# Performance work log

Measured on AMD Instinct MI355X. Metric: run time of the kernel, lower is better.

The kernel has to match this reference:

```python
import jax, jax.numpy as jnp
import numpy as np

B, Z, NOBS = 16384, 64, 2
D = Z + NOBS  # update_mlp_in_size
H1, H2 = 16, 16
HC1, HC2 = 32, 32


def setup_inputs() -> dict:
    key = jax.random.key(0)
    ks = jax.random.split(key, 20)
    inp = {}
    inp['latents'] = jax.random.normal(ks[0], (B, Z), jnp.float32)
    inp['obs'] = jax.random.normal(ks[1], (B, NOBS), jnp.float32)
    # reparameterization noise (torch.randn_like equivalents, made explicit)
    inp['noise_update'] = jax.random.normal(ks[2], (B, D, Z), jnp.float32)
    inp['noise_global'] = jax.random.normal(ks[3], (B, Z), jnp.float32)
    # parameters
    inp['z_0'] = jax.random.normal(ks[4], (Z,), jnp.float32)
    inp['mult_u'] = jnp.ones((D, Z), jnp.float32)
    inp['logvar_u'] = jax.random.uniform(ks[5], (D, Z), jnp.float32, -3.0, -2.0)
    inp['mult_g'] = jnp.ones((Z,), jnp.float32)
    inp['logvar_g'] = jax.random.uniform(ks[6], (Z,), jnp.float32, -3.0, -2.0)
    # per-latent update MLPs, batched over Z
    s = lambda fan_in: 1.0 / np.sqrt(fan_in)
    inp['W1'] = jax.random.uniform(ks[7], (Z, D, H1), jnp.float32, -s(D), s(D))
    inp['b1'] = jax.random.uniform(ks[8], (Z, H1), jnp.float32, -s(D), s(D))
    inp['W2'] = jax.random.uniform(ks[9], (Z, H1, H2), jnp.float32, -s(H1), s(H1))
    inp['b2'] = jax.random.uniform(ks[10], (Z, H2), jnp.float32, -s(H1), s(H1))
    inp['W3'] = jax.random.uniform(ks[11], (Z, H2, 2), jnp.float32, -s(H2), s(H2))
    inp['b3'] = jax.random.uniform(ks[12], (Z, 2), jnp.float32, -s(H2), s(H2))
    # choice MLP (include_stimulus=False -> input dim Z)
    inp['Wc1'] = jax.random.uniform(ks[13], (Z, HC1), jnp.float32, -s(Z), s(Z))
    inp['bc1'] = jax.random.uniform(ks[14], (HC1,), jnp.float32, -s(Z), s(Z))
    inp['Wc2'] = jax.random.uniform(ks[15], (HC1, HC2), jnp.float32, -s(HC1), s(HC1))
    inp['bc2'] = jax.random.uniform(ks[16], (HC2,), jnp.float32, -s(HC1), s(HC1))
    inp['Wc3'] = jax.random.uniform(ks[17], (HC2, 2), jnp.float32, -s(HC2), s(HC2))
    inp['bc3'] = jax.random.uniform(ks[18], (2,), jnp.float32, -s(HC2), s(HC2))
    inp['t_0'] = 0  # False
    return inp


def reference(latents, obs, noise_update, noise_global, z_0, mult_u, logvar_u,
              mult_g, logvar_g, W1, b1, W2, b2, W3, b3,
              Wc1, bc1, Wc2, bc2, Wc3, bc3, t_0):
    lat = jnp.broadcast_to(z_0, latents.shape) if t_0 else latents  # [B,Z]
    x = jnp.concatenate([lat, obs], axis=-1)  # [B,D]
    # --- per-latent update bottlenecks, vectorized over Z ---
    var_u = jnp.exp(logvar_u)                      # [D,Z]
    mean_u = x[:, :, None] * mult_u[None]          # [B,D,Z]
    kld_u = -0.5 * jnp.sum(1.0 + logvar_u[None] - mean_u ** 2 - var_u[None], axis=1)  # [B,Z]
    x_tilde = noise_update * jnp.sqrt(var_u)[None] + mean_u  # [B,D,Z]
    # --- per-latent tiny MLPs, batched as grouped GEMMs ---
    h = jax.nn.relu(jnp.einsum('bdz,zdh->bzh', x_tilde, W1) + b1[None])
    h = jax.nn.relu(jnp.einsum('bzh,zhk->bzk', h, W2) + b2[None])
    o = jnp.einsum('bzk,zko->bzo', h, W3) + b3[None]          # [B,Z,2]
    u = o[..., 0]
    w = jax.nn.sigmoid(o[..., 1])
    new_latents = (1.0 - w) * lat + u * w          # gated update, [B,Z]
    # --- global bottleneck ---
    var_g = jnp.exp(logvar_g)
    mean_g = mult_g * new_latents
    kld_g = -0.5 * jnp.sum(1.0 + logvar_g - mean_g ** 2 - var_g, axis=-1)  # [B]
    z_tilde = noise_global * jnp.sqrt(var_g) + mean_g
    # --- choice MLP (no stimulus) ---
    y = jax.nn.relu(z_tilde @ Wc1 + bc1)
    y = jax.nn.relu(y @ Wc2 + bc2)
    y = y @ Wc3 + bc3                              # [B,2]
    return (y, z_tilde, kld_g, kld_u)
```

## Files before the change

### kernel.cpp

```cpp
#include <hip/hip_runtime.h>
#include <stdint.h>

#define BB 16384
#define ZZ 64
#define DD 66
#define NB 4
#define WPB 4
#define ROWS (WPB*NB)

#define OFF_SVMU 0
#define OFF_C0U  8448
#define OFF_MG   8512
#define OFF_SVG  8576
#define OFF_C0G  8640
#define OFF_W1T  8704
#define OFF_W2T  76288
#define OFF_W3T  92672

__global__ void prep_kernel(const float* __restrict__ mult_u, const float* __restrict__ logvar_u,
                            const float* __restrict__ mult_g, const float* __restrict__ logvar_g,
                            const float* __restrict__ W1, const float* __restrict__ W2,
                            const float* __restrict__ W3, float* __restrict__ ws) {
  const int d = blockIdx.x;
  const int t = threadIdx.x;
  const int z = t >> 2, q = t & 3;

  {
    const float4 v = *reinterpret_cast<const float4*>(W1 + (z*DD + d)*16 + q*4);
    *reinterpret_cast<float4*>(ws + OFF_W1T + ((d*4 + q)*64 + z)*4) = v;
  }
  if (t < ZZ) {
    ws[OFF_SVMU + 2*(d*ZZ + t)]     = mult_u[d*ZZ + t];
    ws[OFF_SVMU + 2*(d*ZZ + t) + 1] = __expf(0.5f * logvar_u[d*ZZ + t]);
  }
  if (d < 16) {
    const float4 v = *reinterpret_cast<const float4*>(W2 + (z*16 + d)*16 + q*4);
    *reinterpret_cast<float4*>(ws + OFF_W2T + ((d*4 + q)*64 + z)*4) = v;
  }
  if (d == 16 || d == 17) {
    const int idx = (d - 16)*256 + t;
    const int qq = idx >> 6, zz = idx & 63;
    const float4 v = *reinterpret_cast<const float4*>(W3 + zz*32 + qq*4);
    *reinterpret_cast<float4*>(ws + OFF_W3T + (qq*64 + zz)*4) = v;
  }
  if (d == 0) {
    if (t < ZZ) {
      float s = 0.f;
      for (int dd = 0; dd < DD; ++dd) {
        const float lv = logvar_u[dd*ZZ + t];
        s += 1.f + lv - __expf(lv);
      }
      ws[OFF_C0U + t] = -0.5f * s;
      ws[OFF_MG  + t] = mult_g[t];
      ws[OFF_SVG + t] = __expf(0.5f * logvar_g[t]);
    }
    if (t == 0) {
      float s = 0.f;
      for (int zc = 0; zc < ZZ; ++zc) {
        const float lv = logvar_g[zc];
        s += 1.f + lv - __expf(lv);
      }
      ws[OFF_C0G] = -0.5f * s;
    }
  }
}

__global__ __launch_bounds__(256, 1)
void disrnn_main(const float* __restrict__ latents, const float* __restrict__ obs,
                 const float* __restrict__ noise_u, const float* __restrict__ noise_g,
                 const float* __restrict__ z0, const float* __restrict__ b1,
                 const float* __restrict__ b2, const float* __restrict__ b3,
                 const float* __restrict__ Wc1, const float* __restrict__ bc1,
                 const float* __restrict__ Wc2, const float* __restrict__ bc2,
                 const float* __restrict__ Wc3, const float* __restrict__ bc3,
                 const float* __restrict__ ws, const int* __restrict__ t0p,
                 float* __restrict__ out) {
  float* out_zt = out + BB*2;
  float* out_kg = out + BB*2 + BB*ZZ;
  float* out_ku = out + BB*2 + BB*ZZ + BB;

  __shared__ float x_lds[WPB][NB][68];
  __shared__ float ztl[ROWS][64];
  __shared__ float y1[ROWS][32];
  __shared__ float y2[ROWS][32];

  const int tid  = threadIdx.x;
  const int w    = tid >> 6;
  const int lane = tid & 63;
  const int b0   = (blockIdx.x * WPB + w) * NB;
  const int t0   = *t0p;

#pragma unroll
  for (int i = 0; i < NB; ++i) {
    x_lds[w][i][lane] = t0 ? z0[lane] : latents[(b0 + i)*ZZ + lane];
    if (lane < 2) x_lds[w][i][ZZ + lane] = obs[(b0 + i)*2 + lane];
  }
  __syncthreads();

  const float c0u_l = ws[OFF_C0U + lane];
  const float mg_l  = ws[OFF_MG + lane];
  const float svg_l = ws[OFF_SVG + lane];
  const float c0g   = ws[OFF_C0G];

  float acc[NB][16], kacc[NB];
  {
    const float4* bp = reinterpret_cast<const float4*>(b1 + lane*16);
    float b1r[16];
#pragma unroll
    for (int q = 0; q < 4; ++q) {
      const float4 v = bp[q];
      b1r[4*q] = v.x; b1r[4*q+1] = v.y; b1r[4*q+2] = v.z; b1r[4*q+3] = v.w;
    }
#pragma unroll
    for (int i = 0; i < NB; ++i) {
      kacc[i] = 0.f;
#pragma unroll
      for (int h = 0; h < 16; ++h) acc[i][h] = b1r[h];
    }
  }

  const float*  w1t  = ws + OFF_W1T;
  const float2* svmu = reinterpret_cast<const float2*>(ws + OFF_SVMU);
  const float* np[NB];
#pragma unroll
  for (int i = 0; i < NB; ++i) np[i] = noise_u + (b0 + i)*DD*ZZ + lane;

  float nv_c[NB], nv_n[NB];
#pragma unroll
  for (int i = 0; i < NB; ++i) { nv_c[i] = np[i][0]; nv_n[i] = np[i][ZZ]; }
  float wv_c[16];
#pragma unroll
  for (int q = 0; q < 4; ++q) {
    const float4 v = *reinterpret_cast<const float4*>(w1t + (q*64 + lane)*4);
    wv_c[4*q] = v.x; wv_c[4*q+1] = v.y; wv_c[4*q+2] = v.z; wv_c[4*q+3] = v.w;
  }
  float2 sm_c = svmu[lane];
  float xv_c[NB];
#pragma unroll
  for (int i = 0; i < NB; ++i) xv_c[i] = x_lds[w][i][0];

#pragma unroll 2
  for (int d = 0; d < DD; ++d) {
    const int dn  = (d + 1 < DD) ? d + 1 : DD - 1;
    const int dnn = (d + 2 < DD) ? d + 2 : DD - 1;
    float nv2[NB];
#pragma unroll
    for (int i = 0; i < NB; ++i) nv2[i] = np[i][dnn*ZZ];
    float wv_n[16];
#pragma unroll
    for (int q = 0; q < 4; ++q) {
      const float4 v = *reinterpret_cast<const float4*>(w1t + ((dn*4 + q)*64 + lane)*4);
      wv_n[4*q] = v.x; wv_n[4*q+1] = v.y; wv_n[4*q+2] = v.z; wv_n[4*q+3] = v.w;
    }
    const float2 sm_n = svmu[dn*ZZ + lane];
    float xv_n[NB];
#pragma unroll
    for (int i = 0; i < NB; ++i) xv_n[i] = x_lds[w][i][dn];

#pragma unroll
    for (int i = 0; i < NB; ++i) {
      const float mean = xv_c[i] * sm_c.x;
      kacc[i] = fmaf(mean, mean, kacc[i]);
      const float xt = fmaf(nv_c[i], sm_c.y, mean);
#pragma unroll
      for (int h = 0; h < 16; ++h) acc[i][h] = fmaf(xt, wv_c[h], acc[i][h]);
    }
#pragma unroll
    for (int i = 0; i < NB; ++i) { nv_c[i] = nv_n[i]; nv_n[i] = nv2[i]; xv_c[i] = xv_n[i]; }
#pragma unroll
    for (int h = 0; h < 16; ++h) wv_c[h] = wv_n[h];
    sm_c = sm_n;
  }

  float h2[NB][16];
  {
    const float4* bp = reinterpret_cast<const float4*>(b2 + lane*16);
    float b2r[16];
#pragma unroll
    for (int q = 0; q < 4; ++q) {
      const float4 v = bp[q];
      b2r[4*q] = v.x; b2r[4*q+1] = v.y; b2r[4*q+2] = v.z; b2r[4*q+3] = v.w;
    }
#pragma unroll
    for (int i = 0; i < NB; ++i) {
#pragma unroll
      for (int h = 0; h < 16; ++h) acc[i][h] = fmaxf(acc[i][h], 0.f);
#pragma unroll
      for (int k = 0; k < 16; ++k) h2[i][k] = b2r[k];
    }
  }
  const float* w2t = ws + OFF_W2T;
#pragma unroll
  for (int h = 0; h < 16; ++h) {
    float wv2[16];
#pragma unroll
    for (int q = 0; q < 4; ++q) {
      const float4 v = *reinterpret_cast<const float4*>(w2t + ((h*4 + q)*64 + lane)*4);
      wv2[4*q] = v.x; wv2[4*q+1] = v.y; wv2[4*q+2] = v.z; wv2[4*q+3] = v.w;
    }
#pragma unroll
    for (int i = 0; i < NB; ++i) {
      const float hv = acc[i][h];
#pragma unroll
      for (int k = 0; k < 16; ++k) h2[i][k] = fmaf(hv, wv2[k], h2[i][k]);
    }
  }

  float w3r[32];
  {
    const float* w3t = ws + OFF_W3T;
#pragma unroll
    for (int q = 0; q < 8; ++q) {
      const float4 v = *reinterpret_cast<const float4*>(w3t + (q*64 + lane)*4);
      w3r[4*q] = v.x; w3r[4*q+1] = v.y; w3r[4*q+2] = v.z; w3r[4*q+3] = v.w;
    }
  }
  const float2 b3v = reinterpret_cast<const float2*>(b3)[lane];
#pragma unroll
  for (int i = 0; i < NB; ++i) {
    const int b = b0 + i;
    float o0 = b3v.x, o1 = b3v.y;
#pragma unroll
    for (int k = 0; k < 16; ++k) {
      const float hv = fmaxf(h2[i][k], 0.f);
      o0 = fmaf(hv, w3r[2*k], o0);
      o1 = fmaf(hv, w3r[2*k + 1], o1);
    }
    const float xl = x_lds[w][i][lane];
    const float wg = 1.f / (1.f + __expf(-o1));
    const float nl = fmaf(wg, o0 - xl, xl);
    const float tg = mg_l * nl;
    const float zt = fmaf(noise_g[b*ZZ + lane], svg_l, tg);
    out_zt[b*ZZ + lane] = zt;
    out_ku[b*ZZ + lane] = fmaf(0.5f, kacc[i], c0u_l);
    ztl[w*NB + i][lane] = zt;
    float t2 = tg * tg;
#pragma unroll
    for (int off = 32; off; off >>= 1) t2 += __shfl_xor(t2, off);
    if (lane == 0) out_kg[b] = fmaf(0.5f, t2, c0g);
  }
  __syncthreads();

  const int r  = tid >> 5;
  const int hc = tid & 31;
#pragma unroll
  for (int g = 0; g < 2; ++g) {
    const int row = g*8 + r;
    float a = bc1[hc];
#pragma unroll
    for (int zc = 0; zc < 64; ++zc) a = fmaf(ztl[row][zc], Wc1[zc*32 + hc], a);
    y1[row][hc] = fmaxf(a, 0.f);
  }
  __syncthreads();
#pragma unroll
  for (int g = 0; g < 2; ++g) {
    const int row = g*8 + r;
    float a = bc2[hc];
#pragma unroll
    for (int k = 0; k < 32; ++k) a = fmaf(y1[row][k], Wc2[k*32 + hc], a);
    y2[row][hc] = fmaxf(a, 0.f);
  }
  __syncthreads();
  if (tid < ROWS*2) {
    const int rr = tid >> 1, o = tid & 1;
    float s = bc3[o];
#pragma unroll
    for (int k = 0; k < 32; ++k) s = fmaf(y2[rr][k], Wc3[2*k + o], s);
    out[(blockIdx.x*ROWS + rr)*2 + o] = s;
  }
}

extern "C" void kernel_launch(void* const* d_in, const int* in_sizes, int n_in,
                              void* d_out, int out_size, void* d_ws, size_t ws_size,
                              hipStream_t stream) {
  (void)in_sizes; (void)n_in; (void)out_size; (void)ws_size;
  const float* latents  = (const float*)d_in[0];
  const float* obs      = (const float*)d_in[1];
  const float* noise_u  = (const float*)d_in[2];
  const float* noise_g  = (const float*)d_in[3];
  const float* z0       = (const float*)d_in[4];
  const float* mult_u   = (const float*)d_in[5];
  const float* logvar_u = (const float*)d_in[6];
  const float* mult_g   = (const float*)d_in[7];
  const float* logvar_g = (const float*)d_in[8];
  const float* W1       = (const float*)d_in[9];
  const float* b1       = (const float*)d_in[10];
  const float* W2       = (const float*)d_in[11];
  const float* b2       = (const float*)d_in[12];
  const float* W3       = (const float*)d_in[13];
  const float* b3       = (const float*)d_in[14];
  const float* Wc1      = (const float*)d_in[15];
  const float* bc1      = (const float*)d_in[16];
  const float* Wc2      = (const float*)d_in[17];
  const float* bc2      = (const float*)d_in[18];
  const float* Wc3      = (const float*)d_in[19];
  const float* bc3      = (const float*)d_in[20];
  const int*  t0p       = (const int*)d_in[21];
  float* ws   = (float*)d_ws;
  float* outp = (float*)d_out;

  prep_kernel<<<66, 256, 0, stream>>>(mult_u, logvar_u, mult_g, logvar_g, W1, W2, W3, ws);
  disrnn_main<<<BB/ROWS, 256, 0, stream>>>(latents, obs, noise_u, noise_g, z0,
                                           b1, b2, b3, Wc1, bc1, Wc2, bc2, Wc3, bc3,
                                           ws, t0p, outp);
}
```

Measured before the change: 503.0 us.

## Stage noise tiles through double-buffered LDS with float4 global loads

Replaces the per-lane scalar noise loads (one 4-byte load per d per row) with wide float4 loads that fetch four d-rows of noise at once. Each chunk is written into a per-wave double-buffered LDS region, then read back as scalars in the compute loop. The main d-loop is restructured into 16 chunks of 4 plus a 2-iteration tail. This cuts the number of global load instructions for the dominant noise stream, at the cost of extra LDS traffic, more LDS usage, and a bounds branch on the prefetch.

New measurement: 500.9 us. No clear change (-0.4%).

```diff
diff --git a/kernel.cpp b/kernel.cpp
--- a/kernel.cpp
+++ b/kernel.cpp
@@ -80,6 +80,7 @@
   float* out_ku = out + BB*2 + BB*ZZ + BB;
 
   __shared__ float x_lds[WPB][NB][68];
+  __shared__ float noise_lds[WPB][2][NB][4*ZZ];
   __shared__ float ztl[ROWS][64];
   __shared__ float y1[ROWS][32];
   __shared__ float y2[ROWS][32];
@@ -121,13 +122,20 @@
 
   const float*  w1t  = ws + OFF_W1T;
   const float2* svmu = reinterpret_cast<const float2*>(ws + OFF_SVMU);
-  const float* np[NB];
-#pragma unroll
-  for (int i = 0; i < NB; ++i) np[i] = noise_u + (b0 + i)*DD*ZZ + lane;
-
-  float nv_c[NB], nv_n[NB];
-#pragma unroll
-  for (int i = 0; i < NB; ++i) { nv_c[i] = np[i][0]; nv_n[i] = np[i][ZZ]; }
+
+  const int dsub = lane >> 4;
+  float4 st[NB];
+  {
+#pragma unroll
+    for (int i = 0; i < NB; ++i)
+      st[i] = *reinterpret_cast<const float4*>(
+          noise_u + ((size_t)(b0 + i)*DD + 0)*ZZ + lane*4);
+#pragma unroll
+    for (int i = 0; i < NB; ++i)
+      *reinterpret_cast<float4*>(&noise_lds[w][0][i][lane*4]) = st[i];
+  }
+  int cur = 0;
+
   float wv_c[16];
 #pragma unroll
   for (int q = 0; q < 4; ++q) {
@@ -139,37 +147,90 @@
 #pragma unroll
   for (int i = 0; i < NB; ++i) xv_c[i] = x_lds[w][i][0];
 
-#pragma unroll 2
-  for (int d = 0; d < DD; ++d) {
-    const int dn  = (d + 1 < DD) ? d + 1 : DD - 1;
-    const int dnn = (d + 2 < DD) ? d + 2 : DD - 1;
-    float nv2[NB];
-#pragma unroll
-    for (int i = 0; i < NB; ++i) nv2[i] = np[i][dnn*ZZ];
-    float wv_n[16];
-#pragma unroll
-    for (int q = 0; q < 4; ++q) {
-      const float4 v = *reinterpret_cast<const float4*>(w1t + ((dn*4 + q)*64 + lane)*4);
-      wv_n[4*q] = v.x; wv_n[4*q+1] = v.y; wv_n[4*q+2] = v.z; wv_n[4*q+3] = v.w;
-    }
-    const float2 sm_n = svmu[dn*ZZ + lane];
-    float xv_n[NB];
-#pragma unroll
-    for (int i = 0; i < NB; ++i) xv_n[i] = x_lds[w][i][dn];
-
-#pragma unroll
-    for (int i = 0; i < NB; ++i) {
-      const float mean = xv_c[i] * sm_c.x;
-      kacc[i] = fmaf(mean, mean, kacc[i]);
-      const float xt = fmaf(nv_c[i], sm_c.y, mean);
-#pragma unroll
-      for (int h = 0; h < 16; ++h) acc[i][h] = fmaf(xt, wv_c[h], acc[i][h]);
-    }
-#pragma unroll
-    for (int i = 0; i < NB; ++i) { nv_c[i] = nv_n[i]; nv_n[i] = nv2[i]; xv_c[i] = xv_n[i]; }
-#pragma unroll
-    for (int h = 0; h < 16; ++h) wv_c[h] = wv_n[h];
-    sm_c = sm_n;
+  for (int c = 0; c < 16; ++c) {
+    {
+      const int d0n = (c + 1) * 4;
+#pragma unroll
+      for (int i = 0; i < NB; ++i) {
+        st[i] = make_float4(0.f, 0.f, 0.f, 0.f);
+        if (d0n + dsub < DD)
+          st[i] = *reinterpret_cast<const float4*>(
+              noise_u + ((size_t)(b0 + i)*DD + d0n)*ZZ + lane*4);
+      }
+    }
+    float nvv[4][NB];
+#pragma unroll
+    for (int j = 0; j < 4; ++j)
+#pragma unroll
+      for (int i = 0; i < NB; ++i)
+        nvv[j][i] = noise_lds[w][cur][i][j*ZZ + lane];
+
+#pragma unroll
+    for (int j = 0; j < 4; ++j) {
+      const int d  = c*4 + j;
+      const int dn = d + 1;
+      float wv_n[16];
+#pragma unroll
+      for (int q = 0; q < 4; ++q) {
+        const float4 v = *reinterpret_cast<const float4*>(w1t + ((dn*4 + q)*64 + lane)*4);
+        wv_n[4*q] = v.x; wv_n[4*q+1] = v.y; wv_n[4*q+2] = v.z; wv_n[4*q+3] = v.w;
+      }
+      const float2 sm_n = svmu[dn*ZZ + lane];
+      float xv_n[NB];
+#pragma unroll
+      for (int i = 0; i < NB; ++i) xv_n[i] = x_lds[w][i][dn];
+#pragma unroll
+      for (int i = 0; i < NB; ++i) {
+        const float mean = xv_c[i] * sm_c.x;
+        kacc[i] = fmaf(mean, mean, kacc[i]);
+        const float xt = fmaf(nvv[j][i], sm_c.y, mean);
+#pragma unroll
+        for (int h = 0; h < 16; ++h) acc[i][h] = fmaf(xt, wv_c[h], acc[i][h]);
+      }
+#pragma unroll
+      for (int h = 0; h < 16; ++h) wv_c[h] = wv_n[h];
+      sm_c = sm_n;
+#pragma unroll
+      for (int i = 0; i < NB; ++i) xv_c[i] = xv_n[i];
+    }
+#pragma unroll
+    for (int i = 0; i < NB; ++i)
+      *reinterpret_cast<float4*>(&noise_lds[w][cur ^ 1][i][lane*4]) = st[i];
+    cur ^= 1;
+  }
+
+  {
+    float nvt[2][NB];
+#pragma unroll
+    for (int j = 0; j < 2; ++j)
+#pragma unroll
+      for (int i = 0; i < NB; ++i)
+        nvt[j][i] = noise_lds[w][cur][i][j*ZZ + lane];
+#pragma unroll
+    for (int j = 0; j < 2; ++j) {
+      const int d  = 64 + j;
+      const int dn = (d + 1 < DD) ? d + 1 : DD - 1;
+      float wv_n[16];
+#pragma unroll
+      for (int q = 0; q < 4; ++q) {
+        const float4 v = *reinterpret_cast<const float4*>(w1t + ((dn*4 + q)*64 + lane)*4);
+        wv_n[4*q] = v.x; wv_n[4*q+1] = v.y; wv_n[4*q+2] = v.z; wv_n[4*q+3] = v.w;
+      }
+      const float2 sm_n = svmu[dn*ZZ + lane];
+#pragma unroll
+      for (int i = 0; i < NB; ++i) {
+        const float mean = xv_c[i] * sm_c.x;
+        kacc[i] = fmaf(mean, mean, kacc[i]);
+        const float xt = fmaf(nvt[j][i], sm_c.y, mean);
+#pragma unroll
+        for (int h = 0; h < 16; ++h) acc[i][h] = fmaf(xt, wv_c[h], acc[i][h]);
+      }
+#pragma unroll
+      for (int h = 0; h < 16; ++h) wv_c[h] = wv_n[h];
+      sm_c = sm_n;
+#pragma unroll
+      for (int i = 0; i < NB; ++i) xv_c[i] = x_lds[w][i][dn];
+    }
   }
 
   float h2[NB][16];
```

## Stage W1 and noise-scale weights through double-buffered LDS chunks

Applied to the files above, without the earlier changes.

Instead of every wave reading the per-d W1 slices and scale/mean vectors directly from global memory, the block cooperatively copies 6-row chunks of W1 and svmu into a double-buffered shared-memory area and computes from LDS while the next chunk is loaded. The goal is to stop four waves from issuing redundant global/L2 loads of the same weights. In exchange it adds a __syncthreads per chunk, about 26KB more LDS per block, and the copy is synchronous, so load latency may not actually be hidden. Noise loads still come straight from global memory and remain the dominant bandwidth cost.

Measured after the change: 533.5 us. +6.1%, slower.

```diff
diff --git a/kernel.cpp b/kernel.cpp
--- a/kernel.cpp
+++ b/kernel.cpp
@@ -7,6 +7,11 @@
 #define NB 4
 #define WPB 4
 #define ROWS (WPB*NB)
+#define CH  6
+#define NCH 11
+#define WCH (CH*4*64*4)
+#define SCH (CH*ZZ*2)
+#define CHF (WCH+SCH)
 
 #define OFF_SVMU 0
 #define OFF_C0U  8448
@@ -80,6 +85,7 @@
   float* out_ku = out + BB*2 + BB*ZZ + BB;
 
   __shared__ float x_lds[WPB][NB][68];
+  __shared__ float wlds[2][CHF];
   __shared__ float ztl[ROWS][64];
   __shared__ float y1[ROWS][32];
   __shared__ float y2[ROWS][32];
@@ -95,6 +101,19 @@
     x_lds[w][i][lane] = t0 ? z0[lane] : latents[(b0 + i)*ZZ + lane];
     if (lane < 2) x_lds[w][i][ZZ + lane] = obs[(b0 + i)*2 + lane];
   }
+
+  const float* w1t = ws + OFF_W1T;
+  const float* svm = ws + OFF_SVMU;
+
+  {
+    const float4* sw = reinterpret_cast<const float4*>(w1t);
+    const float4* sv = reinterpret_cast<const float4*>(svm);
+    float4* dst = reinterpret_cast<float4*>(wlds[0]);
+    for (int t = tid; t < CHF/4; t += 256) {
+      const float4* src = (t < WCH/4) ? (sw + t) : (sv + (t - WCH/4));
+      dst[t] = *src;
+    }
+  }
   __syncthreads();
 
   const float c0u_l = ws[OFF_C0U + lane];
@@ -119,57 +138,71 @@
     }
   }
 
-  const float*  w1t  = ws + OFF_W1T;
-  const float2* svmu = reinterpret_cast<const float2*>(ws + OFF_SVMU);
   const float* np[NB];
 #pragma unroll
-  for (int i = 0; i < NB; ++i) np[i] = noise_u + (b0 + i)*DD*ZZ + lane;
+  for (int i = 0; i < NB; ++i) np[i] = noise_u + (size_t)(b0 + i)*DD*ZZ + lane;
 
   float nv_c[NB], nv_n[NB];
 #pragma unroll
   for (int i = 0; i < NB; ++i) { nv_c[i] = np[i][0]; nv_n[i] = np[i][ZZ]; }
-  float wv_c[16];
-#pragma unroll
-  for (int q = 0; q < 4; ++q) {
-    const float4 v = *reinterpret_cast<const float4*>(w1t + (q*64 + lane)*4);
-    wv_c[4*q] = v.x; wv_c[4*q+1] = v.y; wv_c[4*q+2] = v.z; wv_c[4*q+3] = v.w;
-  }
-  float2 sm_c = svmu[lane];
-  float xv_c[NB];
-#pragma unroll
-  for (int i = 0; i < NB; ++i) xv_c[i] = x_lds[w][i][0];
-
-#pragma unroll 2
-  for (int d = 0; d < DD; ++d) {
-    const int dn  = (d + 1 < DD) ? d + 1 : DD - 1;
-    const int dnn = (d + 2 < DD) ? d + 2 : DD - 1;
-    float nv2[NB];
-#pragma unroll
-    for (int i = 0; i < NB; ++i) nv2[i] = np[i][dnn*ZZ];
-    float wv_n[16];
+
+  int d = 0;
+  for (int c = 0; c < NCH; ++c) {
+    const float* wb = wlds[c & 1];
+    if (c + 1 < NCH) {
+      const float4* sw = reinterpret_cast<const float4*>(w1t + (size_t)(c+1)*WCH);
+      const float4* sv = reinterpret_cast<const float4*>(svm + (size_t)(c+1)*SCH);
+      float4* dst = reinterpret_cast<float4*>(wlds[(c+1) & 1]);
+      for (int t = tid; t < CHF/4; t += 256) {
+        const float4* src = (t < WCH/4) ? (sw + t) : (sv + (t - WCH/4));
+        dst[t] = *src;
+      }
+    }
+    float wv_c[16];
 #pragma unroll
     for (int q = 0; q < 4; ++q) {
-      const float4 v = *reinterpret_cast<const float4*>(w1t + ((dn*4 + q)*64 + lane)*4);
-      wv_n[4*q] = v.x; wv_n[4*q+1] = v.y; wv_n[4*q+2] = v.z; wv_n[4*q+3] = v.w;
-    }
-    const float2 sm_n = svmu[dn*ZZ + lane];
-    float xv_n[NB];
-#pragma unroll
-    for (int i = 0; i < NB; ++i) xv_n[i] = x_lds[w][i][dn];
-
-#pragma unroll
-    for (int i = 0; i < NB; ++i) {
-      const float mean = xv_c[i] * sm_c.x;
-      kacc[i] = fmaf(mean, mean, kacc[i]);
-      const float xt = fmaf(nv_c[i], sm_c.y, mean);
-#pragma unroll
-      for (int h = 0; h < 16; ++h) acc[i][h] = fmaf(xt, wv_c[h], acc[i][h]);
-    }
-#pragma unroll
-    for (int i = 0; i < NB; ++i) { nv_c[i] = nv_n[i]; nv_n[i] = nv2[i]; xv_c[i] = xv_n[i]; }
-#pragma unroll
-    for (int h = 0; h < 16; ++h) wv_c[h] = wv_n[h];
-    sm_c = sm_n;
+      const float4 v = *reinterpret_cast<const float4*>(wb + (q*64 + lane)*4);
+      wv_c[4*q] = v.x; wv_c[4*q+1] = v.y; wv_c[4*q+2] = v.z; wv_c[4*q+3] = v.w;
+    }
+    float2 sm_c = *reinterpret_cast<const float2*>(wb + WCH + lane*2);
+    float xv_c[NB];
+#pragma unroll
+    for (int i = 0; i < NB; ++i) xv_c[i] = x_lds[w][i][d];
+
+#pragma unroll
+    for (int dc = 0; dc < CH; ++dc, ++d) {
+      const int dnn = (d + 2 < DD) ? d + 2 : DD - 1;
+      float nv2[NB];
+#pragma unroll
+      for (int i = 0; i < NB; ++i) nv2[i] = np[i][dnn*ZZ];
+      const int dcn = (dc + 1 < CH) ? dc + 1 : dc;
+      const int dn  = (d + 1 < DD) ? d + 1 : d;
+      float wv_n[16];
+#pragma unroll
+      for (int q = 0; q < 4; ++q) {
+        const float4 v = *reinterpret_cast<const float4*>(wb + ((dcn*4 + q)*64 + lane)*4);
+        wv_n[4*q] = v.x; wv_n[4*q+1] = v.y; wv_n[4*q+2] = v.z; wv_n[4*q+3] = v.w;
+      }
+      const float2 sm_n = *reinterpret_cast<const float2*>(wb + WCH + dcn*128 + lane*2);
+      float xv_n[NB];
+#pragma unroll
+      for (int i = 0; i < NB; ++i) xv_n[i] = x_lds[w][i][dn];
+
+#pragma unroll
+      for (int i = 0; i < NB; ++i) {
+        const float mean = xv_c[i] * sm_c.x;
+        kacc[i] = fmaf(mean, mean, kacc[i]);
+        const float xt = fmaf(nv_c[i], sm_c.y, mean);
+#pragma unroll
+        for (int h = 0; h < 16; ++h) acc[i][h] = fmaf(xt, wv_c[h], acc[i][h]);
+      }
+#pragma unroll
+      for (int i = 0; i < NB; ++i) { nv_c[i] = nv_n[i]; nv_n[i] = nv2[i]; xv_c[i] = xv_n[i]; }
+#pragma unroll
+      for (int h = 0; h < 16; ++h) wv_c[h] = wv_n[h];
+      sm_c = sm_n;
+    }
+    __syncthreads();
   }
 
   float h2[NB][16];
```
